# Optimization experiments

Hardware: AMD Instinct MI355X
Metric: run time of the kernel (lower is better)

## Reference

```python
import jax, jax.numpy as jnp
import numpy as np
from jax import lax

TEMPERATURE = 1.0
STRIDE = 1
PADDING = 1


def setup_inputs() -> dict:
    key = jax.random.key(0)
    ks = jax.random.split(key, 5)
    B, Cin, H, W = 32, 256, 56, 56
    Cout, K, kk = 256, 4, 3
    hidden = Cin // 4
    x = jax.random.normal(ks[0], (B, Cin, H, W), dtype=jnp.float32)
    weight_bank = jax.random.normal(ks[1], (K, Cout, Cin, kk, kk), dtype=jnp.float32) * 0.02
    fc1_w = jax.random.normal(ks[2], (hidden, Cin), dtype=jnp.float32) * (1.0 / np.sqrt(Cin))
    fc1_b = jnp.zeros((hidden,), dtype=jnp.float32)
    fc2_w = jax.random.normal(ks[3], (K, hidden), dtype=jnp.float32) * (1.0 / np.sqrt(hidden))
    fc2_b = jnp.zeros((K,), dtype=jnp.float32)
    return {"x": x, "weight_bank": weight_bank, "fc1_w": fc1_w,
            "fc1_b": fc1_b, "fc2_w": fc2_w, "fc2_b": fc2_b}


def reference(x, weight_bank, fc1_w, fc1_b, fc2_w, fc2_b):
    B, Cin, H, W = x.shape
    K, Cout = weight_bank.shape[0], weight_bank.shape[1]
    kk = weight_bank.shape[3]
    # Router: global average pool -> MLP -> softmax over K banks
    v = jnp.mean(x, axis=(2, 3))                      # [B, Cin]
    h = jax.nn.relu(v @ fc1_w.T + fc1_b)              # [B, hidden]
    logits = h @ fc2_w.T + fc2_b                      # [B, K]
    a = jax.nn.softmax(logits / TEMPERATURE, axis=1)  # [B, K]
    # Per-sample dynamic weight: mix the K banks
    Wdyn = jnp.einsum('bk,kocij->bocij', a, weight_bank)  # [B, Cout, Cin, k, k]
    # Batched per-sample conv via grouped convolution (groups=B)
    x2 = x.reshape(1, B * Cin, H, W)
    W2 = Wdyn.reshape(B * Cout, Cin, kk, kk)
    y = lax.conv_general_dilated(
        x2, W2,
        window_strides=(STRIDE, STRIDE),
        padding=((PADDING, PADDING), (PADDING, PADDING)),
        dimension_numbers=('NCHW', 'OIHW', 'NCHW'),
        feature_group_count=B,
    )
    Ho, Wo = y.shape[2], y.shape[3]
    return y.reshape(B, Cout, Ho, Wo)
```

## Files before the change

kernel.cpp:

```cpp
#include <hip/hip_runtime.h>
#include <stdint.h>

typedef unsigned short u16;
typedef unsigned int   u32;

#define B_SZ  32
#define CIN   256
#define NPIX  3136
#define COUT  256
#define HID   64
#define NBANK 4
#define BANK_SZ 589824
#define WF_N  18874368

#define XROWS 64
#define XSP_N 33554432ull

typedef _Float16 f16x8 __attribute__((ext_vector_type(8)));
typedef short bf16x8 __attribute__((ext_vector_type(8)));
typedef float f32x4  __attribute__((ext_vector_type(4)));

struct __align__(16) U4 { u32 x, y, z, w; };
struct __align__(16) F4 { float x, y, z, w; };

__device__ __forceinline__ float bf2f(u16 u) {
    union { u32 i; float f; } v; v.i = ((u32)u) << 16; return v.f;
}
__device__ __forceinline__ u16 f2bf(float f) {
    union { float f; u32 i; } v; v.f = f;
    u32 u = v.i;
    return (u16)((u + 0x7FFFu + ((u >> 16) & 1u)) >> 16);
}
__device__ __forceinline__ u16 f2h(float f) {
    union { _Float16 h; u16 u; } v; v.h = (_Float16)f;
    return v.u;
}

__device__ __forceinline__ void gload_lds16(const u16* g, u16* l) {
    __builtin_amdgcn_global_load_lds(
        (const __attribute__((address_space(1))) void*)g,
        (__attribute__((address_space(3))) void*)l, 16, 0, 0);
}

__global__ __launch_bounds__(64) void k_mean(const float* __restrict__ x,
                                             float* __restrict__ vout) {
    int bc = blockIdx.x;
    const F4* p = (const F4*)(x + (size_t)bc * NPIX);
    float s = 0.f;
    for (int o = threadIdx.x; o < 784; o += 64) {
        F4 u = p[o];
        s += u.x + u.y + u.z + u.w;
    }
    #pragma unroll
    for (int off = 32; off > 0; off >>= 1) s += __shfl_down(s, off, 64);
    if (threadIdx.x == 0) vout[bc] = s * (1.0f / 3136.0f);
}

__global__ __launch_bounds__(64) void k_router(const float* __restrict__ v,
        const float* __restrict__ fc1w, const float* __restrict__ fc1b,
        const float* __restrict__ fc2w, const float* __restrict__ fc2b,
        float* __restrict__ aout) {
    int b = blockIdx.x, j = threadIdx.x;
    __shared__ float hl[HID];
    __shared__ float lg[NBANK];
    const float* vb = v + b * CIN;
    float acc = fc1b[j];
    const F4* wrow = (const F4*)(fc1w + j * CIN);
    for (int o = 0; o < 64; ++o) {
        F4 u = wrow[o];
        acc += vb[o * 4 + 0] * u.x + vb[o * 4 + 1] * u.y
             + vb[o * 4 + 2] * u.z + vb[o * 4 + 3] * u.w;
    }
    hl[j] = acc > 0.f ? acc : 0.f;
    __syncthreads();
    if (j < NBANK) {
        float l = fc2b[j];
        for (int t = 0; t < HID; ++t) l += hl[t] * fc2w[j * HID + t];
        lg[j] = l;
    }
    __syncthreads();
    if (j == 0) {
        float m = lg[0];
        for (int k = 1; k < NBANK; ++k) m = fmaxf(m, lg[k]);
        float e[NBANK], se = 0.f;
        for (int k = 0; k < NBANK; ++k) { e[k] = expf(lg[k] - m); se += e[k]; }
        for (int k = 0; k < NBANK; ++k) aout[b * NBANK + k] = e[k] / se;
    }
}

__global__ __launch_bounds__(256) void k_split(const float* __restrict__ x,
                                               u16* __restrict__ xsp) {
    const int blk = blockIdx.x;
    const int row = blk & 63;
    const int bc  = blk >> 6;
    const int b   = bc >> 3, cis = bc & 7;
    const int t   = threadIdx.x;
    const size_t obase = (size_t)blk * 2048;
    const int hin = row - 1;
    if (hin < 0 || hin >= 56) {
        U4 z; z.x = 0; z.y = 0; z.z = 0; z.w = 0;
        *(U4*)(xsp + obase + (size_t)t * 8) = z;
        return;
    }
    __shared__ float ls[32 * 57];
    const float* xb = x + ((size_t)b * CIN + cis * 32) * NPIX + hin * 56;
    for (int idx = t; idx < 448; idx += 256) {
        int ci = idx / 14, o = idx - ci * 14;
        F4 u = *(const F4*)(xb + (size_t)ci * NPIX + o * 4);
        float* d = &ls[ci * 57 + o * 4];
        d[0] = u.x; d[1] = u.y; d[2] = u.z; d[3] = u.w;
    }
    __syncthreads();
    const int ci2 = (t & 15) * 2;
    const int cg  = t >> 4;
    const int ciq = ci2 >> 3;
    const int cil = ci2 & 7;
    #pragma unroll
    for (int k = 0; k < 4; ++k) {
        int col = cg + k * 16;
        int win = col - 1;
        float v0 = 0.f, v1 = 0.f;
        if (win >= 0 && win < 56) {
            v0 = ls[ci2 * 57 + win];
            v1 = ls[(ci2 + 1) * 57 + win];
        }
        size_t pos = obase + (size_t)(ciq * 64 + col) * 8 + cil;
        *(u32*)(xsp + pos) = (u32)f2h(v0) | ((u32)f2h(v1) << 16);
    }
}

#define PM_PAD 145
__global__ __launch_bounds__(256) void k_premix(const float* __restrict__ bank,
        const float* __restrict__ aws, u16* __restrict__ wf) {
    int cof   = blockIdx.x >> 4;
    int cis16 = blockIdx.x & 15;
    int bgrp  = blockIdx.y;
    __shared__ float lw[64 * PM_PAD];
    for (int idx = threadIdx.x; idx < 64 * 144; idx += 256) {
        int s = idx / 144;
        int e = idx - s * 144;
        int k = s >> 4, co_l = s & 15;
        lw[s * PM_PAD + e] =
            bank[(size_t)(k * COUT + cof * 16 + co_l) * (CIN * 9) + cis16 * 144 + e];
    }
    __syncthreads();
    const int cis   = cis16 >> 1;
    const int qbase = (cis16 & 1) * 2;
    for (int b8 = 0; b8 < 8; ++b8) {
        const int b = bgrp * 8 + b8;
        float a0 = aws[b * 4 + 0], a1 = aws[b * 4 + 1];
        float a2 = aws[b * 4 + 2], a3 = aws[b * 4 + 3];
        for (int o = threadIdx.x; o < 288; o += 256) {
            int t  = o >> 5;
            int hlane = o & 31;
            int lane  = qbase * 16 + hlane;
            int m = lane & 15, q = lane >> 4;
            int q_loc = q - qbase;
            u16 ph[8];
            #pragma unroll
            for (int jj = 0; jj < 8; ++jj) {
                int ee = (q_loc * 8 + jj) * 9 + t;
                float w = a0 * lw[(0 * 16 + m) * PM_PAD + ee]
                        + a1 * lw[(1 * 16 + m) * PM_PAD + ee]
                        + a2 * lw[(2 * 16 + m) * PM_PAD + ee]
                        + a3 * lw[(3 * 16 + m) * PM_PAD + ee];
                ph[jj] = f2h(w);
            }
            size_t off = ((((size_t)b * 16 + cof) * 9 + t) * 8 + cis) * 512
                       + (size_t)lane * 8;
            U4 uh;
            uh.x = (u32)ph[0] | ((u32)ph[1] << 16);
            uh.y = (u32)ph[2] | ((u32)ph[3] << 16);
            uh.z = (u32)ph[4] | ((u32)ph[5] << 16);
            uh.w = (u32)ph[6] | ((u32)ph[7] << 16);
            *(U4*)(wf + off) = uh;
        }
    }
}

__global__ __launch_bounds__(256, 2) void k_conv2(
        const u16* __restrict__ wf,
        const u16* __restrict__ xsp,
        float* __restrict__ out) {
    __shared__ u16 xbuf[2][16384];

    const int flat = blockIdx.x;
    const int g    = flat & 7;
    const int idx  = flat >> 3;
    const int b    = g * 4 + (idx / 26);
    const int r    = idx % 26;
    const int coblk = r / 13;
    const int pt    = r % 13;

    const int tid  = threadIdx.x;
    const int wave = tid >> 6;
    const int lane = tid & 63;
    const int wm = wave >> 1, wn = wave & 1;

    const int pix0 = pt * 256;
    const int h0   = pix0 / 56;

    const size_t rowbase = (((size_t)b * 8) * 64 + h0) * 2048;

    int bb[8], pl[8];
    #pragma unroll
    for (int nf = 0; nf < 8; ++nf) {
        int p = pix0 + wn * 128 + nf * 16 + (lane & 15);
        pl[nf] = p;
        int pc = p < NPIX ? p : NPIX - 1;
        int hp = pc / 56, wp = pc - (pc / 56) * 56;
        bb[nf] = ((hp - h0) * 256 + (lane >> 4) * 64 + wp) * 16;
    }

    const u16* wbase = wf
        + ((size_t)b * 16 + coblk * 8 + wm * 4) * (9 * 8 * 512)
        + (size_t)lane * 8;

    f32x4 acc[4][8];
    #pragma unroll
    for (int i = 0; i < 4; ++i)
        #pragma unroll
        for (int j = 0; j < 8; ++j) { f32x4 z = {0.f, 0.f, 0.f, 0.f}; acc[i][j] = z; }

    {
        const u16* sb = xsp + rowbase;
        #pragma unroll
        for (int c = wave; c < 32; c += 4)
            gload_lds16(sb + c * 512 + lane * 8, &xbuf[0][c * 512 + lane * 8]);
    }

    for (int cis = 0; cis < 8; ++cis) {
        asm volatile("s_waitcnt vmcnt(0) lgkmcnt(0)" ::: "memory");
        __builtin_amdgcn_s_barrier();
        __builtin_amdgcn_sched_barrier(0);
        if (cis < 7) {
            const u16* sb = xsp + rowbase + (size_t)(cis + 1) * 131072;
            u16* db = &xbuf[(cis + 1) & 1][0];
            #pragma unroll
            for (int c = wave; c < 32; c += 4)
                gload_lds16(sb + c * 512 + lane * 8, db + c * 512 + lane * 8);
        }
        __builtin_amdgcn_sched_barrier(0);

        const char* xb = (const char*)&xbuf[cis & 1][0];
        f16x8 w[3][4];
        #pragma unroll
        for (int mf = 0; mf < 4; ++mf) {
            w[0][mf] = *(const f16x8*)(wbase + (size_t)((mf * 9 + 0) * 8 + cis) * 512);
            w[1][mf] = *(const f16x8*)(wbase + (size_t)((mf * 9 + 1) * 8 + cis) * 512);
        }
        #pragma unroll
        for (int t = 0; t < 9; ++t) {
            if (t < 7) {
                #pragma unroll
                for (int mf = 0; mf < 4; ++mf)
                    w[(t + 2) % 3][mf] =
                        *(const f16x8*)(wbase + (size_t)((mf * 9 + t + 2) * 8 + cis) * 512);
            }
            const int ty = t / 3, tx = t - ty * 3;
            const int toff = ty * 4096 + tx * 16;
            __builtin_amdgcn_s_setprio(1);
            #pragma unroll
            for (int nf = 0; nf < 8; ++nf) {
                f16x8 bx = *(const f16x8*)(xb + bb[nf] + toff);
                #pragma unroll
                for (int mf = 0; mf < 4; ++mf) {
                    acc[mf][nf] = __builtin_amdgcn_mfma_f32_16x16x32_f16(
                        w[t % 3][mf], bx, acc[mf][nf], 0, 0, 0);
                }
            }
            __builtin_amdgcn_s_setprio(0);
        }
    }

    float* ob = out + (size_t)b * COUT * NPIX;
    #pragma unroll
    for (int mf = 0; mf < 4; ++mf) {
        int cobase = coblk * 128 + wm * 64 + mf * 16 + (lane >> 4) * 4;
        #pragma unroll
        for (int nf = 0; nf < 8; ++nf) {
            int p = pl[nf];
            if (p < NPIX) {
                #pragma unroll
                for (int r = 0; r < 4; ++r)
                    ob[(size_t)(cobase + r) * NPIX + p] = acc[mf][nf][r];
            }
        }
    }
}

__global__ __launch_bounds__(256, 2) void k_conv_fb(const float* __restrict__ x,
        const float* __restrict__ bank,
        const float* __restrict__ aws,
        float* __restrict__ out) {
    const int pt    = blockIdx.x;
    const int coblk = blockIdx.y;
    const int b     = blockIdx.z;

    const int tid  = threadIdx.x;
    const int wave = tid >> 6;
    const int lane = tid & 63;
    const int wm = wave >> 1, wn = wave & 1;

    __shared__ u16 xs[2][6 * 58 * 32];

    const int pix0 = pt * 128;
    const int h0   = pix0 / 56;
    const int rlo  = h0 - 1;

    const float* xb = x + (size_t)b * CIN * NPIX;

    int bbase[4], pl[4];
    #pragma unroll
    for (int nf = 0; nf < 4; ++nf) {
        int p = pix0 + wn * 64 + nf * 16 + (lane & 15);
        pl[nf] = p;
        int pc = p < NPIX ? p : NPIX - 1;
        int hp = pc / 56, wp = pc - (pc / 56) * 56;
        bbase[nf] = ((hp - h0) * 58 + wp) * 64 + (lane >> 4) * 16;
    }

    float a0 = aws[b * 4 + 0], a1 = aws[b * 4 + 1];
    float a2 = aws[b * 4 + 2], a3 = aws[b * 4 + 3];

    f32x4 acc[4][4];
    #pragma unroll
    for (int i = 0; i < 4; ++i)
        #pragma unroll
        for (int j = 0; j < 4; ++j) { f32x4 z = {0.f, 0.f, 0.f, 0.f}; acc[i][j] = z; }

    for (int cis = 0; cis < 8; ++cis) {
        const int ci0 = cis * 32;
        __syncthreads();
        for (int idx = tid; idx < 1392; idx += 256) {
            int oct = idx / 348;
            int rc  = idx - oct * 348;
            int row = rc / 58, col = rc - row * 58;
            int hin = rlo + row, win = col - 1;
            U4 uh; uh.x = 0; uh.y = 0; uh.z = 0; uh.w = 0;
            U4 ul = uh;
            if (hin >= 0 && hin < 56 && win >= 0 && win < 56) {
                const float* gp = xb + (size_t)(ci0 + oct * 8) * NPIX + hin * 56 + win;
                u16 eh[8], el[8];
                #pragma unroll
                for (int i = 0; i < 8; ++i) {
                    float v = gp[(size_t)i * NPIX];
                    u16 h = f2bf(v);
                    eh[i] = h;
                    el[i] = f2bf(v - bf2f(h));
                }
                uh.x = (u32)eh[0] | ((u32)eh[1] << 16);
                uh.y = (u32)eh[2] | ((u32)eh[3] << 16);
                uh.z = (u32)eh[4] | ((u32)eh[5] << 16);
                uh.w = (u32)eh[6] | ((u32)eh[7] << 16);
                ul.x = (u32)el[0] | ((u32)el[1] << 16);
                ul.y = (u32)el[2] | ((u32)el[3] << 16);
                ul.z = (u32)el[4] | ((u32)el[5] << 16);
                ul.w = (u32)el[6] | ((u32)el[7] << 16);
            }
            *(U4*)(&xs[0][rc * 32 + oct * 8]) = uh;
            *(U4*)(&xs[1][rc * 32 + oct * 8]) = ul;
        }
        __syncthreads();

        #pragma unroll
        for (int t = 0; t < 9; ++t) {
            const int ty = t / 3, tx = t - (t / 3) * 3;
            bf16x8 ah[4], al[4];
            #pragma unroll
            for (int mf = 0; mf < 4; ++mf) {
                int co = coblk * 128 + wm * 64 + mf * 16 + (lane & 15);
                int q = lane >> 4;
                u16 ph[8], plo[8];
                #pragma unroll
                for (int jj = 0; jj < 8; ++jj) {
                    int ci = ci0 + q * 8 + jj;
                    size_t base = ((size_t)co * CIN + ci) * 9 + t;
                    float w = a0 * bank[base]
                            + a1 * bank[base + BANK_SZ]
                            + a2 * bank[base + 2 * BANK_SZ]
                            + a3 * bank[base + 3 * BANK_SZ];
                    u16 h = f2bf(w);
                    ph[jj]  = h;
                    plo[jj] = f2bf(w - bf2f(h));
                }
                union { U4 u; bf16x8 v; } pu;
                pu.u.x = (u32)ph[0] | ((u32)ph[1] << 16);
                pu.u.y = (u32)ph[2] | ((u32)ph[3] << 16);
                pu.u.z = (u32)ph[4] | ((u32)ph[5] << 16);
                pu.u.w = (u32)ph[6] | ((u32)ph[7] << 16);
                ah[mf] = pu.v;
                pu.u.x = (u32)plo[0] | ((u32)plo[1] << 16);
                pu.u.y = (u32)plo[2] | ((u32)plo[3] << 16);
                pu.u.z = (u32)plo[4] | ((u32)plo[5] << 16);
                pu.u.w = (u32)plo[6] | ((u32)plo[7] << 16);
                al[mf] = pu.v;
            }
            const int toff = (ty * 58 + tx) * 64;
            #pragma unroll
            for (int nf = 0; nf < 4; ++nf) {
                bf16x8 bh = *(const bf16x8*)((const char*)&xs[0][0] + bbase[nf] + toff);
                bf16x8 bl = *(const bf16x8*)((const char*)&xs[1][0] + bbase[nf] + toff);
                #pragma unroll
                for (int mf = 0; mf < 4; ++mf) {
                    acc[mf][nf] = __builtin_amdgcn_mfma_f32_16x16x32_bf16(
                        ah[mf], bh, acc[mf][nf], 0, 0, 0);
                    acc[mf][nf] = __builtin_amdgcn_mfma_f32_16x16x32_bf16(
                        ah[mf], bl, acc[mf][nf], 0, 0, 0);
                    acc[mf][nf] = __builtin_amdgcn_mfma_f32_16x16x32_bf16(
                        al[mf], bh, acc[mf][nf], 0, 0, 0);
                }
            }
        }
    }

    float* ob = out + (size_t)b * COUT * NPIX;
    #pragma unroll
    for (int mf = 0; mf < 4; ++mf) {
        int cobase = coblk * 128 + wm * 64 + mf * 16 + (lane >> 4) * 4;
        #pragma unroll
        for (int nf = 0; nf < 4; ++nf) {
            int p = pl[nf];
            if (p < NPIX) {
                #pragma unroll
                for (int r = 0; r < 4; ++r)
                    ob[(size_t)(cobase + r) * NPIX + p] = acc[mf][nf][r];
            }
        }
    }
}

extern "C" void kernel_launch(void* const* d_in, const int* in_sizes, int n_in,
                              void* d_out, int out_size, void* d_ws, size_t ws_size,
                              hipStream_t stream) {
    const float* x    = (const float*)d_in[0];
    const float* bank = (const float*)d_in[1];
    const float* fc1w = (const float*)d_in[2];
    const float* fc1b = (const float*)d_in[3];
    const float* fc2w = (const float*)d_in[4];
    const float* fc2b = (const float*)d_in[5];
    float* out = (float*)d_out;

    float* a_ws = (float*)d_ws;
    float* v_ws = (float*)d_ws + 128;
    u16*   wf   = (u16*)((char*)d_ws + 65536);
    u16*   xsp  = (u16*)((char*)d_ws + 65536 + (size_t)WF_N * sizeof(u16));

    const size_t need = (size_t)65536 + (size_t)WF_N * sizeof(u16)
                      + (size_t)XSP_N * sizeof(u16);

    k_mean<<<dim3(B_SZ * CIN), dim3(64), 0, stream>>>(x, v_ws);
    k_router<<<dim3(B_SZ), dim3(64), 0, stream>>>(v_ws, fc1w, fc1b, fc2w, fc2b, a_ws);

    if (ws_size >= need) {
        k_premix<<<dim3(256, 4), dim3(256), 0, stream>>>(bank, a_ws, wf);
        k_split<<<dim3(B_SZ * 8 * XROWS), dim3(256), 0, stream>>>(x, xsp);
        k_conv2<<<dim3(832), dim3(256), 0, stream>>>(wf, xsp, out);
    } else {
        k_conv_fb<<<dim3(25, 2, B_SZ), dim3(256), 0, stream>>>(x, bank, a_ws, out);
    }
}
```

Measured before the change: 349.4 us.

## Fuse channel-mean into split kernel and widen premix grid and weight prefetch

The global-average-pool reduction moves into the fp16 split kernel, which writes per-row partial sums; a new router kernel reduces those partials, so the separate k_mean pass over x is dropped. Premix now runs on twice as many blocks with fewer batches each, and the conv inner loop prefetches weights three taps ahead with a four-slot register ring instead of two ahead with three. This removes a full read of x and the serialised mean launch, at the cost of an extra partial-sum buffer in the workspace and more registers in the conv kernel.

```diff
diff --git a/kernel.cpp b/kernel.cpp
--- a/kernel.cpp
+++ b/kernel.cpp
@@ -88,8 +88,52 @@
     }
 }
 
+__global__ __launch_bounds__(64) void k_router2(const float* __restrict__ vpart,
+        const float* __restrict__ fc1w, const float* __restrict__ fc1b,
+        const float* __restrict__ fc2w, const float* __restrict__ fc2b,
+        float* __restrict__ aout) {
+    int b = blockIdx.x, j = threadIdx.x;
+    __shared__ float vsh[CIN];
+    __shared__ float hl[HID];
+    __shared__ float lg[NBANK];
+    #pragma unroll
+    for (int c4 = 0; c4 < 4; ++c4) {
+        int ci  = c4 * 64 + j;
+        int cis = ci >> 5, cil = ci & 31;
+        const float* p = vpart + ((size_t)(b * 8 + cis) * 64) * 32 + cil;
+        float s = 0.f;
+        #pragma unroll
+        for (int row = 0; row < 64; ++row) s += p[row * 32];
+        vsh[ci] = s * (1.0f / 3136.0f);
+    }
+    __syncthreads();
+    float acc = fc1b[j];
+    const F4* wrow = (const F4*)(fc1w + j * CIN);
+    for (int o = 0; o < 64; ++o) {
+        F4 u = wrow[o];
+        acc += vsh[o * 4 + 0] * u.x + vsh[o * 4 + 1] * u.y
+             + vsh[o * 4 + 2] * u.z + vsh[o * 4 + 3] * u.w;
+    }
+    hl[j] = acc > 0.f ? acc : 0.f;
+    __syncthreads();
+    if (j < NBANK) {
+        float l = fc2b[j];
+        for (int t = 0; t < HID; ++t) l += hl[t] * fc2w[j * HID + t];
+        lg[j] = l;
+    }
+    __syncthreads();
+    if (j == 0) {
+        float m = lg[0];
+        for (int k = 1; k < NBANK; ++k) m = fmaxf(m, lg[k]);
+        float e[NBANK], se = 0.f;
+        for (int k = 0; k < NBANK; ++k) { e[k] = expf(lg[k] - m); se += e[k]; }
+        for (int k = 0; k < NBANK; ++k) aout[b * NBANK + k] = e[k] / se;
+    }
+}
+
 __global__ __launch_bounds__(256) void k_split(const float* __restrict__ x,
-                                               u16* __restrict__ xsp) {
+                                               u16* __restrict__ xsp,
+                                               float* __restrict__ vpart) {
     const int blk = blockIdx.x;
     const int row = blk & 63;
     const int bc  = blk >> 6;
@@ -100,6 +144,7 @@
     if (hin < 0 || hin >= 56) {
         U4 z; z.x = 0; z.y = 0; z.z = 0; z.w = 0;
         *(U4*)(xsp + obase + (size_t)t * 8) = z;
+        if (t < 32) vpart[(size_t)blk * 32 + t] = 0.f;
         return;
     }
     __shared__ float ls[32 * 57];
@@ -111,6 +156,15 @@
         d[0] = u.x; d[1] = u.y; d[2] = u.z; d[3] = u.w;
     }
     __syncthreads();
+    {
+        int ci = t >> 3, part = t & 7;
+        const float* r = &ls[ci * 57 + part * 7];
+        float s = r[0] + r[1] + r[2] + r[3] + r[4] + r[5] + r[6];
+        s += __shfl_down(s, 4, 64);
+        s += __shfl_down(s, 2, 64);
+        s += __shfl_down(s, 1, 64);
+        if (part == 0) vpart[(size_t)blk * 32 + ci] = s;
+    }
     const int ci2 = (t & 15) * 2;
     const int cg  = t >> 4;
     const int ciq = ci2 >> 3;
@@ -146,8 +200,8 @@
     __syncthreads();
     const int cis   = cis16 >> 1;
     const int qbase = (cis16 & 1) * 2;
-    for (int b8 = 0; b8 < 8; ++b8) {
-        const int b = bgrp * 8 + b8;
+    for (int b4 = 0; b4 < 4; ++b4) {
+        const int b = bgrp * 4 + b4;
         float a0 = aws[b * 4 + 0], a1 = aws[b * 4 + 1];
         float a2 = aws[b * 4 + 2], a3 = aws[b * 4 + 3];
         for (int o = threadIdx.x; o < 288; o += 256) {
@@ -243,19 +297,20 @@
         __builtin_amdgcn_sched_barrier(0);
 
         const char* xb = (const char*)&xbuf[cis & 1][0];
-        f16x8 w[3][4];
+        f16x8 w[4][4];
         #pragma unroll
         for (int mf = 0; mf < 4; ++mf) {
             w[0][mf] = *(const f16x8*)(wbase + (size_t)((mf * 9 + 0) * 8 + cis) * 512);
             w[1][mf] = *(const f16x8*)(wbase + (size_t)((mf * 9 + 1) * 8 + cis) * 512);
+            w[2][mf] = *(const f16x8*)(wbase + (size_t)((mf * 9 + 2) * 8 + cis) * 512);
         }
         #pragma unroll
         for (int t = 0; t < 9; ++t) {
-            if (t < 7) {
+            if (t < 6) {
                 #pragma unroll
                 for (int mf = 0; mf < 4; ++mf)
-                    w[(t + 2) % 3][mf] =
-                        *(const f16x8*)(wbase + (size_t)((mf * 9 + t + 2) * 8 + cis) * 512);
+                    w[(t + 3) & 3][mf] =
+                        *(const f16x8*)(wbase + (size_t)((mf * 9 + t + 3) * 8 + cis) * 512);
             }
             const int ty = t / 3, tx = t - ty * 3;
             const int toff = ty * 4096 + tx * 16;
@@ -266,7 +321,7 @@
                 #pragma unroll
                 for (int mf = 0; mf < 4; ++mf) {
                     acc[mf][nf] = __builtin_amdgcn_mfma_f32_16x16x32_f16(
-                        w[t % 3][mf], bx, acc[mf][nf], 0, 0, 0);
+                        w[t & 3][mf], bx, acc[mf][nf], 0, 0, 0);
                 }
             }
             __builtin_amdgcn_s_setprio(0);
@@ -445,18 +500,21 @@
     float* v_ws = (float*)d_ws + 128;
     u16*   wf   = (u16*)((char*)d_ws + 65536);
     u16*   xsp  = (u16*)((char*)d_ws + 65536 + (size_t)WF_N * sizeof(u16));
+    float* vpart = (float*)((char*)d_ws + 65536 + (size_t)WF_N * sizeof(u16)
+                            + (size_t)XSP_N * sizeof(u16));
 
     const size_t need = (size_t)65536 + (size_t)WF_N * sizeof(u16)
-                      + (size_t)XSP_N * sizeof(u16);
-
-    k_mean<<<dim3(B_SZ * CIN), dim3(64), 0, stream>>>(x, v_ws);
-    k_router<<<dim3(B_SZ), dim3(64), 0, stream>>>(v_ws, fc1w, fc1b, fc2w, fc2b, a_ws);
+                      + (size_t)XSP_N * sizeof(u16)
+                      + (size_t)B_SZ * 8 * XROWS * 32 * sizeof(float);
 
     if (ws_size >= need) {
-        k_premix<<<dim3(256, 4), dim3(256), 0, stream>>>(bank, a_ws, wf);
-        k_split<<<dim3(B_SZ * 8 * XROWS), dim3(256), 0, stream>>>(x, xsp);
+        k_split<<<dim3(B_SZ * 8 * XROWS), dim3(256), 0, stream>>>(x, xsp, vpart);
+        k_router2<<<dim3(B_SZ), dim3(64), 0, stream>>>(vpart, fc1w, fc1b, fc2w, fc2b, a_ws);
+        k_premix<<<dim3(256, 8), dim3(256), 0, stream>>>(bank, a_ws, wf);
         k_conv2<<<dim3(832), dim3(256), 0, stream>>>(wf, xsp, out);
     } else {
+        k_mean<<<dim3(B_SZ * CIN), dim3(64), 0, stream>>>(x, v_ws);
+        k_router<<<dim3(B_SZ), dim3(64), 0, stream>>>(v_ws, fc1w, fc1b, fc2w, fc2b, a_ws);
         k_conv_fb<<<dim3(25, 2, B_SZ), dim3(256), 0, stream>>>(x, bank, a_ws, out);
     }
 }
```

Measured after the change: 410.3 us. +17.4%, slower.
